# Performance work log

Hardware: AMD Instinct MI355X
Metric: run time of the kernel (lower is better)

The kernel has to match this reference:

```python
import jax, jax.numpy as jnp
import numpy as np

# Mamba-1.4B-like dims
BATCH, SEQ, HID = 1, 2048, 2048
INTER, STATE, DT_RANK, KCONV = 4096, 16, 128, 4


def setup_inputs() -> dict:
    key = jax.random.key(0)
    ks = jax.random.split(key, 8)
    f = jnp.float32
    return {
        "input_states": jax.random.normal(ks[0], (BATCH, SEQ, HID), f),
        "in_proj_w": jax.random.normal(ks[1], (HID, 2 * INTER), f) * (HID ** -0.5),
        "conv_w": jax.random.normal(ks[2], (INTER, 1, KCONV), f) * (KCONV ** -0.5),  # (O, I/groups=1, K) depthwise
        "conv_b": jnp.zeros((INTER,), f),
        "x_proj_w": jax.random.normal(ks[3], (INTER, DT_RANK + 2 * STATE), f) * (INTER ** -0.5),
        "dt_proj_w": jax.random.normal(ks[4], (DT_RANK, INTER), f) * (DT_RANK ** -0.5),
        "dt_proj_b": jax.random.normal(ks[5], (INTER,), f) * 0.1,
        "A_log": jnp.log(jnp.broadcast_to(jnp.arange(1, STATE + 1, dtype=f), (INTER, STATE))),
        "D": jnp.ones((INTER,), f),
        "out_proj_w": jax.random.normal(ks[6], (INTER, HID), f) * (INTER ** -0.5),
    }


def _mamba_forward(input_states, in_proj_w, conv_w, conv_b, x_proj_w,
                   dt_proj_w, dt_proj_b, A_log, D, out_proj_w):
    Bsz, L, _ = input_states.shape
    Idim, _, K = conv_w.shape
    N = A_log.shape[1]
    R = dt_proj_w.shape[0]

    proj = input_states @ in_proj_w                       # (B, L, 2I)
    hidden, gate = jnp.split(proj, 2, axis=-1)            # each (B, L, I)

    # depthwise causal conv over sequence (pad K-1, keep first L outputs)
    xc = jnp.swapaxes(hidden, 1, 2)                       # (B, I, L)
    xc = jax.lax.conv_general_dilated(
        xc, conv_w, window_strides=(1,), padding=((K - 1, K - 1),),
        feature_group_count=Idim)
    xc = xc[:, :, :L] + conv_b[None, :, None]
    u = jax.nn.silu(jnp.swapaxes(xc, 1, 2))               # (B, L, I)

    # input-dependent SSM params
    ssm_in = u @ x_proj_w                                 # (B, L, R + 2N)
    dt_in, Bc, Cc = jnp.split(ssm_in, [R, R + N], axis=-1)
    dt = jax.nn.softplus(dt_in @ dt_proj_w + dt_proj_b)   # (B, L, I)
    A = -jnp.exp(A_log)                                   # (I, N)

    def step(state, xs):
        dt_t, B_t, C_t, u_t = xs                          # (B,I) (B,N) (B,N) (B,I)
        dA = jnp.exp(dt_t[:, :, None] * A[None])          # (B, I, N)
        state = state * dA + (dt_t * u_t)[:, :, None] * B_t[:, None, :]
        y_t = jnp.einsum('bin,bn->bi', state, C_t)
        return state, y_t

    xs = (jnp.swapaxes(dt, 0, 1), jnp.swapaxes(Bc, 0, 1),
          jnp.swapaxes(Cc, 0, 1), jnp.swapaxes(u, 0, 1))
    state0 = jnp.zeros((Bsz, Idim, N), dt.dtype)
    _, ys = jax.lax.scan(step, state0, xs)                # (L, B, I)
    y = jnp.swapaxes(ys, 0, 1)                            # (B, L, I)

    y = (y + u * D) * jax.nn.silu(gate)
    return y @ out_proj_w                                 # (B, L, H)


def reference(input_states, in_proj_w, conv_w, conv_b, x_proj_w,
              dt_proj_w, dt_proj_b, A_log, D, out_proj_w):
    return _mamba_forward(input_states, in_proj_w, conv_w, conv_b, x_proj_w,
                          dt_proj_w, dt_proj_b, A_log, D, out_proj_w)
```

## Files before the change

kernel.cpp:

```cpp
#include <hip/hip_runtime.h>
#include <stdint.h>

#define LSEQ 2048
#define HID  2048
#define IDIM 4096
#define NSTATE 16
#define RRANK 128
#define GDIM 160

#define GCHUNK 64
#define TCHUNK (LSEQ / GCHUNK)

typedef _Float16 f16x8 __attribute__((ext_vector_type(8)));
typedef _Float16 f16x2 __attribute__((ext_vector_type(2)));
typedef float f32x4 __attribute__((ext_vector_type(4)));

#define GLOAD_LDS16(g, l) __builtin_amdgcn_global_load_lds( \
    (const __attribute__((address_space(1))) void*)(g),     \
    (__attribute__((address_space(3))) void*)(l), 16, 0, 0)

__device__ __forceinline__ float softplus_f(float x) {
    if (x > 20.f) return x;
    return log1pf(__expf(x));
}
__device__ __forceinline__ float silu_f(float x) {
    return x / (1.f + __expf(-x));
}

__device__ __forceinline__ void transpose_tile(const float* __restrict__ in,
                                               _Float16* __restrict__ out,
                                               int R, int C, int tr, int tc,
                                               _Float16 (*tile)[66]) {
    const int c0 = tc * 64, r0 = tr * 64;
    const int t = threadIdx.x;
    const int tx = t & 15, ty = t >> 4;
    const int ox = t & 7, oy = t >> 3;
    const bool full = (c0 + 64 <= C) && (r0 + 64 <= R);
    if (full) {
        #pragma unroll
        for (int j = 0; j < 4; ++j) {
            int r = ty + j * 16;
            float4 v = *(const float4*)(in + (long)(r0 + r) * C + c0 + tx * 4);
            tile[r][tx * 4 + 0] = (_Float16)v.x;
            tile[r][tx * 4 + 1] = (_Float16)v.y;
            tile[r][tx * 4 + 2] = (_Float16)v.z;
            tile[r][tx * 4 + 3] = (_Float16)v.w;
        }
        __syncthreads();
        #pragma unroll
        for (int j = 0; j < 2; ++j) {
            int c = oy + j * 32;
            f16x8 v;
            #pragma unroll
            for (int e = 0; e < 8; ++e) v[e] = tile[ox * 8 + e][c];
            *(f16x8*)(out + (long)(c0 + c) * R + r0 + ox * 8) = v;
        }
    } else {
        #pragma unroll
        for (int j = 0; j < 4; ++j) {
            int r = ty + j * 16;
            #pragma unroll
            for (int e = 0; e < 4; ++e) {
                int c = c0 + tx * 4 + e;
                float v = (r0 + r < R && c < C) ? in[(long)(r0 + r) * C + c] : 0.f;
                tile[r][tx * 4 + e] = (_Float16)v;
            }
        }
        __syncthreads();
        #pragma unroll
        for (int j = 0; j < 2; ++j) {
            int c = c0 + oy + j * 32;
            if (c < C) {
                #pragma unroll
                for (int e = 0; e < 8; ++e) {
                    int r = r0 + ox * 8 + e;
                    if (r < R) out[(long)c * R + r] = tile[ox * 8 + e][oy + j * 32];
                }
            }
        }
    }
}

__global__ __launch_bounds__(256)
void prep_kernel(const float* __restrict__ x_in, const float* __restrict__ w_in,
                 const float* __restrict__ xw, const float* __restrict__ dtw,
                 const float* __restrict__ ow,
                 _Float16* __restrict__ Xf, _Float16* __restrict__ Wt1,
                 _Float16* __restrict__ Wt2, _Float16* __restrict__ Wt3,
                 _Float16* __restrict__ Wt4) {
    __shared__ _Float16 tile[64][66];
    int b = blockIdx.x;
    if (b < 4096) { transpose_tile(w_in, Wt1, HID, 2 * IDIM, b / 128, b % 128, tile); return; }
    b -= 4096;
    if (b < 192) { transpose_tile(xw, Wt2, IDIM, GDIM, b / 3, b % 3, tile); return; }
    b -= 192;
    if (b < 128) { transpose_tile(dtw, Wt3, RRANK, IDIM, b / 64, b % 64, tile); return; }
    b -= 128;
    if (b < 2048) { transpose_tile(ow, Wt4, IDIM, HID, b / 32, b % 32, tile); return; }
    b -= 2048;
    long base = (long)b * 4096 + threadIdx.x * 16;
    #pragma unroll
    for (int h = 0; h < 2; ++h) {
        float4 a = *(const float4*)(x_in + base + h * 8);
        float4 c = *(const float4*)(x_in + base + h * 8 + 4);
        f16x8 v;
        v[0] = (_Float16)a.x; v[1] = (_Float16)a.y; v[2] = (_Float16)a.z; v[3] = (_Float16)a.w;
        v[4] = (_Float16)c.x; v[5] = (_Float16)c.y; v[6] = (_Float16)c.z; v[7] = (_Float16)c.w;
        *(f16x8*)(Xf + base + h * 8) = v;
    }
}

#define BM 128
#define BK 64

template <typename CT, int BN_, bool SOFTPLUS>
__global__ __launch_bounds__(256)
void gemm_bt_kernel(const _Float16* __restrict__ A, const _Float16* __restrict__ Bt,
                    CT* __restrict__ C, int M, int N, int K, int kc,
                    const float* __restrict__ bias) {
    constexpr int NI = BN_ / 32;
    constexpr int NISS_B = BN_ * 8 / 256;
    __shared__ _Float16 As[BM * BK];
    __shared__ _Float16 Bs[BN_ * BK];
    const int m0 = blockIdx.y * BM;
    const int n0 = blockIdx.x * BN_;
    const int t = threadIdx.x;
    const int wave = t >> 6;
    const int lane = t & 63;
    const int wm = wave >> 1, wn = wave & 1;
    const int lrow = lane & 15;
    const int quad = lane >> 4;
    const int sw8 = (lrow & 7) * 8;

    f32x4 acc[4][NI];
    #pragma unroll
    for (int mi = 0; mi < 4; ++mi)
        #pragma unroll
        for (int ni = 0; ni < NI; ++ni)
            #pragma unroll
            for (int r = 0; r < 4; ++r)
                acc[mi][ni][r] = 0.f;

    const int k_begin = blockIdx.z * kc;
    const _Float16* pA[4];
    #pragma unroll
    for (int j = 0; j < 4; ++j) {
        int s = j * 256 + t;
        int row = s >> 3;
        int ch = (s & 7) ^ (row & 7);
        pA[j] = A + (long)(m0 + row) * K + ch * 8 + k_begin;
    }
    const _Float16* pB[NISS_B];
    #pragma unroll
    for (int j = 0; j < NISS_B; ++j) {
        int s = j * 256 + t;
        int row = s >> 3;
        int ch = (s & 7) ^ (row & 7);
        pB[j] = Bt + (long)(n0 + row) * K + ch * 8 + k_begin;
    }

    for (int kk = 0; kk < kc; kk += BK) {
        #pragma unroll
        for (int j = 0; j < 4; ++j) {
            GLOAD_LDS16(pA[j], As + (j * 256 + wave * 64) * 8);
            pA[j] += BK;
        }
        #pragma unroll
        for (int j = 0; j < NISS_B; ++j) {
            GLOAD_LDS16(pB[j], Bs + (j * 256 + wave * 64) * 8);
            pB[j] += BK;
        }
        __syncthreads();

        #pragma unroll
        for (int h = 0; h < 2; ++h) {
            const int qoff = (h * 32 + quad * 8) ^ sw8;
            f16x8 af[4], bf[NI];
            #pragma unroll
            for (int mi = 0; mi < 4; ++mi)
                af[mi] = *(const f16x8*)(As + (wm * 64 + mi * 16 + lrow) * BK + qoff);
            #pragma unroll
            for (int ni = 0; ni < NI; ++ni)
                bf[ni] = *(const f16x8*)(Bs + (wn * (BN_ / 2) + ni * 16 + lrow) * BK + qoff);
            #pragma unroll
            for (int mi = 0; mi < 4; ++mi)
                #pragma unroll
                for (int ni = 0; ni < NI; ++ni)
                    acc[mi][ni] = __builtin_amdgcn_mfma_f32_16x16x32_f16(af[mi], bf[ni], acc[mi][ni], 0, 0, 0);
        }
        __syncthreads();
    }

    CT* Cz = C + (long)blockIdx.z * M * N;
    #pragma unroll
    for (int mi = 0; mi < 4; ++mi) {
        #pragma unroll
        for (int ni = 0; ni < NI; ++ni) {
            int col = n0 + wn * (BN_ / 2) + ni * 16 + lrow;
            if (col < N) {
                float bv = SOFTPLUS ? bias[col] : 0.f;
                #pragma unroll
                for (int r = 0; r < 4; ++r) {
                    int row = m0 + wm * 64 + mi * 16 + quad * 4 + r;
                    float v = acc[mi][ni][r];
                    if (SOFTPLUS) v = softplus_f(v + bv);
                    Cz[(long)row * N + col] = (CT)v;
                }
            }
        }
    }
}

__global__ void xproj_reduce_kernel(const float* __restrict__ part, float* __restrict__ ssm,
                                    _Float16* __restrict__ dtin) {
    int idx = blockIdx.x * 256 + threadIdx.x;
    if (idx >= LSEQ * GDIM) return;
    int t = idx / GDIM;
    int c = idx - t * GDIM;
    float v = 0.f;
    #pragma unroll
    for (int k = 0; k < 8; ++k)
        v += part[((long)k * LSEQ + t) * 256 + c];
    ssm[idx] = v;
    if (c < RRANK) dtin[t * RRANK + c] = (_Float16)v;
}

__global__ void opart_reduce_kernel(const float* __restrict__ part, float* __restrict__ out) {
    int idx = blockIdx.x * 256 + threadIdx.x;
    float4 a = ((const float4*)part)[idx];
    float4 b = ((const float4*)(part + (long)LSEQ * HID))[idx];
    ((float4*)out)[idx] = make_float4(a.x + b.x, a.y + b.y, a.z + b.z, a.w + b.w);
}

__global__ void conv_silu_kernel(const _Float16* __restrict__ proj, const float* __restrict__ w,
                                 const float* __restrict__ b, _Float16* __restrict__ u16) {
    int idx = blockIdx.x * 256 + threadIdx.x;
    int i0 = (idx & 511) * 8;
    int t0 = (idx >> 9) * 4;
    f16x8 r[7];
    #pragma unroll
    for (int k = 0; k < 7; ++k) {
        int tt = t0 - 3 + k;
        if (tt >= 0) r[k] = *(const f16x8*)(proj + (long)tt * (2 * IDIM) + i0);
        else         r[k] = f16x8{0,0,0,0,0,0,0,0};
    }
    float4 wv[8]; float bb[8];
    #pragma unroll
    for (int j = 0; j < 8; ++j) { wv[j] = ((const float4*)w)[i0 + j]; bb[j] = b[i0 + j]; }
    #pragma unroll
    for (int tt = 0; tt < 4; ++tt) {
        f16x8 res;
        #pragma unroll
        for (int j = 0; j < 8; ++j) {
            float a = bb[j] + (float)r[tt][j] * wv[j].x + (float)r[tt+1][j] * wv[j].y
                            + (float)r[tt+2][j] * wv[j].z + (float)r[tt+3][j] * wv[j].w;
            res[j] = (_Float16)(a / (1.f + __expf(-a)));
        }
        *(f16x8*)(u16 + (long)(t0 + tt) * IDIM + i0) = res;
    }
}

__global__ __launch_bounds__(256)
void scan_pass1_kernel(const _Float16* __restrict__ dtf, const float* __restrict__ ssm,
                       const _Float16* __restrict__ u16, const float* __restrict__ A_log,
                       _Float16* __restrict__ Pc, _Float16* __restrict__ Sc) {
    const int c = blockIdx.y;
    const int i0 = (blockIdx.x * 256 + threadIdx.x) * 2;

    __shared__ float Bs[TCHUNK * 16];
    for (int idx = threadIdx.x; idx < TCHUNK * 16; idx += 256) {
        int t = idx >> 4, n = idx & 15;
        Bs[idx] = ssm[(c * TCHUNK + t) * GDIM + RRANK + n];
    }
    __syncthreads();

    float A[2][16];
    #pragma unroll
    for (int ch = 0; ch < 2; ++ch) {
        const float4* Ap = (const float4*)(A_log + (long)(i0 + ch) * 16);
        #pragma unroll
        for (int q = 0; q < 4; ++q) {
            float4 v = Ap[q];
            A[ch][q * 4 + 0] = -__expf(v.x);
            A[ch][q * 4 + 1] = -__expf(v.y);
            A[ch][q * 4 + 2] = -__expf(v.z);
            A[ch][q * 4 + 3] = -__expf(v.w);
        }
    }

    float s[2][16], pr[2][16];
    #pragma unroll
    for (int ch = 0; ch < 2; ++ch)
        #pragma unroll
        for (int n = 0; n < 16; ++n) { s[ch][n] = 0.f; pr[ch][n] = 1.f; }

    long base = (long)c * TCHUNK * IDIM + i0;
    for (int t = 0; t < TCHUNK; ++t) {
        f16x2 dt2 = *(const f16x2*)(dtf + base + (long)t * IDIM);
        f16x2 u2  = *(const f16x2*)(u16 + base + (long)t * IDIM);
        #pragma unroll
        for (int ch = 0; ch < 2; ++ch) {
            float dt = (float)dt2[ch];
            float dtu = dt * (float)u2[ch];
            #pragma unroll
            for (int n = 0; n < 16; ++n) {
                float dA = __expf(dt * A[ch][n]);
                s[ch][n] = s[ch][n] * dA + dtu * Bs[t * 16 + n];
                pr[ch][n] *= dA;
            }
        }
    }

    long o = ((long)c * IDIM + i0) * 16;
    #pragma unroll
    for (int ch = 0; ch < 2; ++ch) {
        #pragma unroll
        for (int q = 0; q < 2; ++q) {
            f16x8 pv, sv;
            #pragma unroll
            for (int e = 0; e < 8; ++e) {
                pv[e] = (_Float16)pr[ch][q * 8 + e];
                sv[e] = (_Float16)s[ch][q * 8 + e];
            }
            *(f16x8*)(Pc + o + ch * 16 + q * 8) = pv;
            *(f16x8*)(Sc + o + ch * 16 + q * 8) = sv;
        }
    }
}

__global__ void scan_combine_kernel(const _Float16* __restrict__ Pc, _Float16* __restrict__ ScInit) {
    int tid = blockIdx.x * 256 + threadIdx.x;
    const long stride = (long)IDIM * 16;
    const long off = (long)tid * 2;
    f16x2 p4[4], s4[4];
    #pragma unroll
    for (int k = 0; k < 4; ++k) {
        p4[k] = *(const f16x2*)(Pc + (long)k * stride + off);
        s4[k] = *(const f16x2*)(ScInit + (long)k * stride + off);
    }
    float c0 = 0.f, c1 = 0.f;
    for (int g = 0; g < GCHUNK / 4; ++g) {
        f16x2 pc[4], sc[4];
        #pragma unroll
        for (int k = 0; k < 4; ++k) { pc[k] = p4[k]; sc[k] = s4[k]; }
        if (g + 1 < GCHUNK / 4) {
            #pragma unroll
            for (int k = 0; k < 4; ++k) {
                long o2 = (long)((g + 1) * 4 + k) * stride + off;
                p4[k] = *(const f16x2*)(Pc + o2);
                s4[k] = *(const f16x2*)(ScInit + o2);
            }
        }
        #pragma unroll
        for (int k = 0; k < 4; ++k) {
            long o = (long)(g * 4 + k) * stride + off;
            *(f16x2*)(ScInit + o) = f16x2{(_Float16)c0, (_Float16)c1};
            c0 = c0 * (float)pc[k][0] + (float)sc[k][0];
            c1 = c1 * (float)pc[k][1] + (float)sc[k][1];
        }
    }
}

__global__ __launch_bounds__(256)
void scan_pass3_kernel(const _Float16* __restrict__ dtf, const float* __restrict__ ssm,
                       const _Float16* __restrict__ u16, const _Float16* __restrict__ proj,
                       const float* __restrict__ A_log, const float* __restrict__ Dp,
                       const _Float16* __restrict__ Init, _Float16* __restrict__ y16) {
    const int c = blockIdx.y;
    const int i0 = (blockIdx.x * 256 + threadIdx.x) * 2;

    __shared__ float Bs[TCHUNK * 16];
    __shared__ float Cs[TCHUNK * 16];
    for (int idx = threadIdx.x; idx < TCHUNK * 16; idx += 256) {
        int t = idx >> 4, n = idx & 15;
        Bs[idx] = ssm[(c * TCHUNK + t) * GDIM + RRANK + n];
        Cs[idx] = ssm[(c * TCHUNK + t) * GDIM + RRANK + NSTATE + n];
    }
    __syncthreads();

    float A[2][16];
    #pragma unroll
    for (int ch = 0; ch < 2; ++ch) {
        const float4* Ap = (const float4*)(A_log + (long)(i0 + ch) * 16);
        #pragma unroll
        for (int q = 0; q < 4; ++q) {
            float4 v = Ap[q];
            A[ch][q * 4 + 0] = -__expf(v.x);
            A[ch][q * 4 + 1] = -__expf(v.y);
            A[ch][q * 4 + 2] = -__expf(v.z);
            A[ch][q * 4 + 3] = -__expf(v.w);
        }
    }
    float2 Dv = *(const float2*)(Dp + i0);

    float s[2][16];
    {
        long o = ((long)c * IDIM + i0) * 16;
        #pragma unroll
        for (int ch = 0; ch < 2; ++ch)
            #pragma unroll
            for (int q = 0; q < 2; ++q) {
                f16x8 v = *(const f16x8*)(Init + o + ch * 16 + q * 8);
                #pragma unroll
                for (int e = 0; e < 8; ++e) s[ch][q * 8 + e] = (float)v[e];
            }
    }

    long base = (long)c * TCHUNK * IDIM + i0;
    for (int t = 0; t < TCHUNK; ++t) {
        f16x2 dt2 = *(const f16x2*)(dtf + base + (long)t * IDIM);
        f16x2 u2  = *(const f16x2*)(u16 + base + (long)t * IDIM);
        int tg = c * TCHUNK + t;
        f16x2 g2 = *(const f16x2*)(proj + (long)tg * (2 * IDIM) + IDIM + i0);
        f16x2 res;
        #pragma unroll
        for (int ch = 0; ch < 2; ++ch) {
            float dt = (float)dt2[ch];
            float uv = (float)u2[ch];
            float dtu = dt * uv;
            float y = 0.f;
            #pragma unroll
            for (int n = 0; n < 16; ++n) {
                float dA = __expf(dt * A[ch][n]);
                s[ch][n] = s[ch][n] * dA + dtu * Bs[t * 16 + n];
                y += s[ch][n] * Cs[t * 16 + n];
            }
            float g = (float)g2[ch];
            float Dch = ch ? Dv.y : Dv.x;
            res[ch] = (_Float16)((y + uv * Dch) * silu_f(g));
        }
        *(f16x2*)(y16 + base + (long)t * IDIM) = res;
    }
}

extern "C" void kernel_launch(void* const* d_in, const int* in_sizes, int n_in,
                              void* d_out, int out_size, void* d_ws, size_t ws_size,
                              hipStream_t stream) {
    const float* x_in  = (const float*)d_in[0];
    const float* w_in  = (const float*)d_in[1];
    const float* cw    = (const float*)d_in[2];
    const float* cb    = (const float*)d_in[3];
    const float* xw    = (const float*)d_in[4];
    const float* dtw   = (const float*)d_in[5];
    const float* dtb   = (const float*)d_in[6];
    const float* alog  = (const float*)d_in[7];
    const float* Dp    = (const float*)d_in[8];
    const float* ow    = (const float*)d_in[9];
    float* out = (float*)d_out;

    char* p = (char*)d_ws;
    auto alloc = [&](size_t bytes) { char* r = p; p += (bytes + 255) & ~255ull; return r; };
    _Float16* Xf    = (_Float16*)alloc((size_t)LSEQ * HID * 2);
    _Float16* Wt1   = (_Float16*)alloc((size_t)2 * IDIM * HID * 2);
    _Float16* proj  = (_Float16*)alloc((size_t)LSEQ * 2 * IDIM * 2);
    _Float16* u16   = (_Float16*)alloc((size_t)LSEQ * IDIM * 2);
    _Float16* Wt2   = (_Float16*)alloc((size_t)256 * IDIM * 2);
    float*    ssm   = (float*)alloc((size_t)LSEQ * GDIM * 4);
    _Float16* dtin  = (_Float16*)alloc((size_t)LSEQ * RRANK * 2);
    _Float16* Wt3   = (_Float16*)alloc((size_t)IDIM * RRANK * 2);
    _Float16* dtf   = (_Float16*)alloc((size_t)LSEQ * IDIM * 2);
    _Float16* Wt4   = (_Float16*)alloc((size_t)HID * IDIM * 2);
    _Float16* y16   = (_Float16*)alloc((size_t)LSEQ * IDIM * 2);

    float* xpart = (float*)Wt1;
    _Float16* Pc = (_Float16*)Wt1;
    _Float16* Sc = Pc + (size_t)GCHUNK * IDIM * 16;
    float* opart = (float*)Wt1;

    prep_kernel<<<7488, 256, 0, stream>>>(x_in, w_in, xw, dtw, ow, Xf, Wt1, Wt2, Wt3, Wt4);
    gemm_bt_kernel<_Float16, 128, false><<<dim3(2 * IDIM / 128, LSEQ / BM, 1), 256, 0, stream>>>(
        Xf, Wt1, proj, LSEQ, 2 * IDIM, HID, HID, nullptr);
    conv_silu_kernel<<<(LSEQ / 4) * (IDIM / 8) / 256, 256, 0, stream>>>(proj, cw, cb, u16);
    gemm_bt_kernel<float, 128, false><<<dim3(2, LSEQ / BM, 8), 256, 0, stream>>>(
        u16, Wt2, xpart, LSEQ, 256, IDIM, IDIM / 8, nullptr);
    xproj_reduce_kernel<<<(LSEQ * GDIM + 255) / 256, 256, 0, stream>>>(xpart, ssm, dtin);
    gemm_bt_kernel<_Float16, 128, true><<<dim3(IDIM / 128, LSEQ / BM, 1), 256, 0, stream>>>(
        dtin, Wt3, dtf, LSEQ, IDIM, RRANK, RRANK, dtb);
    scan_pass1_kernel<<<dim3(IDIM / 512, GCHUNK), 256, 0, stream>>>(
        dtf, ssm, u16, alog, Pc, Sc);
    scan_combine_kernel<<<(IDIM * NSTATE / 2) / 256, 256, 0, stream>>>(Pc, Sc);
    scan_pass3_kernel<<<dim3(IDIM / 512, GCHUNK), 256, 0, stream>>>(
        dtf, ssm, u16, proj, alog, Dp, Sc, y16);
    gemm_bt_kernel<float, 128, false><<<dim3(HID / 128, LSEQ / BM, 2), 256, 0, stream>>>(
        y16, Wt4, opart, LSEQ, HID, IDIM, IDIM / 2, nullptr);
    opart_reduce_kernel<<<(LSEQ * HID / 4) / 256, 256, 0, stream>>>(opart, out);
}
```

Before: 470.6 us.

## Fuse pipeline stages into fewer kernels using software grid barriers

Merges the conv into the in-projection GEMM, the x-proj split-K reduction into its GEMM, the three scan passes into one kernel, and the out-proj reduction into its GEMM, each joined by an atomic-counter grid barrier. It also replaces the per-step running product of decay factors with a single exp of the summed dt, and stores out-proj partials in fp16. The goal is to cut kernel launch overhead and intermediate traffic. The catch is that the barriers need every block resident at once (1024 blocks for in-proj), which can deadlock or serialize. The fp16 partials also lower accuracy.

```diff
diff --git a/kernel.cpp b/kernel.cpp
--- a/kernel.cpp
+++ b/kernel.cpp
@@ -25,6 +25,17 @@
 }
 __device__ __forceinline__ float silu_f(float x) {
     return x / (1.f + __expf(-x));
+}
+
+__device__ __forceinline__ void grid_barrier(int* cnt, int expected) {
+    __syncthreads();
+    if (threadIdx.x == 0) {
+        __threadfence();
+        atomicAdd(cnt, 1);
+        while (__hip_atomic_load(cnt, __ATOMIC_ACQUIRE, __HIP_MEMORY_SCOPE_AGENT) < expected)
+            __builtin_amdgcn_s_sleep(2);
+    }
+    __syncthreads();
 }
 
 __device__ __forceinline__ void transpose_tile(const float* __restrict__ in,
@@ -87,9 +98,10 @@
                  const float* __restrict__ ow,
                  _Float16* __restrict__ Xf, _Float16* __restrict__ Wt1,
                  _Float16* __restrict__ Wt2, _Float16* __restrict__ Wt3,
-                 _Float16* __restrict__ Wt4) {
+                 _Float16* __restrict__ Wt4, int* __restrict__ ctr) {
     __shared__ _Float16 tile[64][66];
     int b = blockIdx.x;
+    if (b == 0 && threadIdx.x < 8) ctr[threadIdx.x] = 0;
     if (b < 4096) { transpose_tile(w_in, Wt1, HID, 2 * IDIM, b / 128, b % 128, tile); return; }
     b -= 4096;
     if (b < 192) { transpose_tile(xw, Wt2, IDIM, GDIM, b / 3, b % 3, tile); return; }
@@ -113,17 +125,14 @@
 #define BM 128
 #define BK 64
 
-template <typename CT, int BN_, bool SOFTPLUS>
-__global__ __launch_bounds__(256)
-void gemm_bt_kernel(const _Float16* __restrict__ A, const _Float16* __restrict__ Bt,
-                    CT* __restrict__ C, int M, int N, int K, int kc,
-                    const float* __restrict__ bias) {
-    constexpr int NI = BN_ / 32;
-    constexpr int NISS_B = BN_ * 8 / 256;
-    __shared__ _Float16 As[BM * BK];
-    __shared__ _Float16 Bs[BN_ * BK];
+template <typename CT, bool SOFTPLUS>
+__device__ __forceinline__
+void gemm_core(const _Float16* __restrict__ A, const _Float16* __restrict__ Bt,
+               CT* __restrict__ C, int M, int N, int K, int kc,
+               const float* __restrict__ bias,
+               _Float16* __restrict__ As, _Float16* __restrict__ Bs) {
     const int m0 = blockIdx.y * BM;
-    const int n0 = blockIdx.x * BN_;
+    const int n0 = blockIdx.x * 128;
     const int t = threadIdx.x;
     const int wave = t >> 6;
     const int lane = t & 63;
@@ -132,30 +141,24 @@
     const int quad = lane >> 4;
     const int sw8 = (lrow & 7) * 8;
 
-    f32x4 acc[4][NI];
+    f32x4 acc[4][4];
     #pragma unroll
     for (int mi = 0; mi < 4; ++mi)
         #pragma unroll
-        for (int ni = 0; ni < NI; ++ni)
+        for (int ni = 0; ni < 4; ++ni)
             #pragma unroll
             for (int r = 0; r < 4; ++r)
                 acc[mi][ni][r] = 0.f;
 
     const int k_begin = blockIdx.z * kc;
     const _Float16* pA[4];
+    const _Float16* pB[4];
     #pragma unroll
     for (int j = 0; j < 4; ++j) {
         int s = j * 256 + t;
         int row = s >> 3;
         int ch = (s & 7) ^ (row & 7);
         pA[j] = A + (long)(m0 + row) * K + ch * 8 + k_begin;
-    }
-    const _Float16* pB[NISS_B];
-    #pragma unroll
-    for (int j = 0; j < NISS_B; ++j) {
-        int s = j * 256 + t;
-        int row = s >> 3;
-        int ch = (s & 7) ^ (row & 7);
         pB[j] = Bt + (long)(n0 + row) * K + ch * 8 + k_begin;
     }
 
@@ -164,9 +167,6 @@
         for (int j = 0; j < 4; ++j) {
             GLOAD_LDS16(pA[j], As + (j * 256 + wave * 64) * 8);
             pA[j] += BK;
-        }
-        #pragma unroll
-        for (int j = 0; j < NISS_B; ++j) {
             GLOAD_LDS16(pB[j], Bs + (j * 256 + wave * 64) * 8);
             pB[j] += BK;
         }
@@ -175,17 +175,17 @@
         #pragma unroll
         for (int h = 0; h < 2; ++h) {
             const int qoff = (h * 32 + quad * 8) ^ sw8;
-            f16x8 af[4], bf[NI];
+            f16x8 af[4], bf[4];
             #pragma unroll
             for (int mi = 0; mi < 4; ++mi)
                 af[mi] = *(const f16x8*)(As + (wm * 64 + mi * 16 + lrow) * BK + qoff);
             #pragma unroll
-            for (int ni = 0; ni < NI; ++ni)
-                bf[ni] = *(const f16x8*)(Bs + (wn * (BN_ / 2) + ni * 16 + lrow) * BK + qoff);
+            for (int ni = 0; ni < 4; ++ni)
+                bf[ni] = *(const f16x8*)(Bs + (wn * 64 + ni * 16 + lrow) * BK + qoff);
             #pragma unroll
             for (int mi = 0; mi < 4; ++mi)
                 #pragma unroll
-                for (int ni = 0; ni < NI; ++ni)
+                for (int ni = 0; ni < 4; ++ni)
                     acc[mi][ni] = __builtin_amdgcn_mfma_f32_16x16x32_f16(af[mi], bf[ni], acc[mi][ni], 0, 0, 0);
         }
         __syncthreads();
@@ -195,8 +195,8 @@
     #pragma unroll
     for (int mi = 0; mi < 4; ++mi) {
         #pragma unroll
-        for (int ni = 0; ni < NI; ++ni) {
-            int col = n0 + wn * (BN_ / 2) + ni * 16 + lrow;
+        for (int ni = 0; ni < 4; ++ni) {
+            int col = n0 + wn * 64 + ni * 16 + lrow;
             if (col < N) {
                 float bv = SOFTPLUS ? bias[col] : 0.f;
                 #pragma unroll
@@ -211,30 +211,19 @@
     }
 }
 
-__global__ void xproj_reduce_kernel(const float* __restrict__ part, float* __restrict__ ssm,
-                                    _Float16* __restrict__ dtin) {
-    int idx = blockIdx.x * 256 + threadIdx.x;
-    if (idx >= LSEQ * GDIM) return;
-    int t = idx / GDIM;
-    int c = idx - t * GDIM;
-    float v = 0.f;
-    #pragma unroll
-    for (int k = 0; k < 8; ++k)
-        v += part[((long)k * LSEQ + t) * 256 + c];
-    ssm[idx] = v;
-    if (c < RRANK) dtin[t * RRANK + c] = (_Float16)v;
-}
-
-__global__ void opart_reduce_kernel(const float* __restrict__ part, float* __restrict__ out) {
-    int idx = blockIdx.x * 256 + threadIdx.x;
-    float4 a = ((const float4*)part)[idx];
-    float4 b = ((const float4*)(part + (long)LSEQ * HID))[idx];
-    ((float4*)out)[idx] = make_float4(a.x + b.x, a.y + b.y, a.z + b.z, a.w + b.w);
-}
-
-__global__ void conv_silu_kernel(const _Float16* __restrict__ proj, const float* __restrict__ w,
-                                 const float* __restrict__ b, _Float16* __restrict__ u16) {
-    int idx = blockIdx.x * 256 + threadIdx.x;
+__global__ __launch_bounds__(256, 4)
+void inproj_conv_kernel(const _Float16* __restrict__ Xf, const _Float16* __restrict__ Wt1,
+                        _Float16* __restrict__ proj, const float* __restrict__ cw,
+                        const float* __restrict__ cb, _Float16* __restrict__ u16,
+                        int* __restrict__ ctr) {
+    __shared__ _Float16 As[BM * BK];
+    __shared__ _Float16 Bs[128 * BK];
+    gemm_core<_Float16, false>(Xf, Wt1, proj, LSEQ, 2 * IDIM, HID, HID, nullptr, As, Bs);
+
+    grid_barrier(ctr, 1024);
+
+    int bid = blockIdx.y * gridDim.x + blockIdx.x;
+    int idx = bid * 256 + threadIdx.x;
     int i0 = (idx & 511) * 8;
     int t0 = (idx >> 9) * 4;
     f16x8 r[7];
@@ -246,7 +235,7 @@
     }
     float4 wv[8]; float bb[8];
     #pragma unroll
-    for (int j = 0; j < 8; ++j) { wv[j] = ((const float4*)w)[i0 + j]; bb[j] = b[i0 + j]; }
+    for (int j = 0; j < 8; ++j) { wv[j] = ((const float4*)cw)[i0 + j]; bb[j] = cb[i0 + j]; }
     #pragma unroll
     for (int tt = 0; tt < 4; ++tt) {
         f16x8 res;
@@ -261,16 +250,78 @@
 }
 
 __global__ __launch_bounds__(256)
-void scan_pass1_kernel(const _Float16* __restrict__ dtf, const float* __restrict__ ssm,
-                       const _Float16* __restrict__ u16, const float* __restrict__ A_log,
-                       _Float16* __restrict__ Pc, _Float16* __restrict__ Sc) {
-    const int c = blockIdx.y;
-    const int i0 = (blockIdx.x * 256 + threadIdx.x) * 2;
-
-    __shared__ float Bs[TCHUNK * 16];
+void xproj_kernel(const _Float16* __restrict__ u16, const _Float16* __restrict__ Wt2,
+                  float* __restrict__ xpart, float* __restrict__ ssm,
+                  _Float16* __restrict__ dtin, int* __restrict__ ctr) {
+    __shared__ _Float16 As[BM * BK];
+    __shared__ _Float16 Bs[128 * BK];
+    gemm_core<float, false>(u16, Wt2, xpart, LSEQ, 256, IDIM, IDIM / 8, nullptr, As, Bs);
+
+    grid_barrier(ctr, 256);
+
+    int bid = (blockIdx.z * gridDim.y + blockIdx.y) * gridDim.x + blockIdx.x;
+    for (int k = bid * 256 + threadIdx.x; k < LSEQ * GDIM; k += 256 * 256) {
+        int t = k / GDIM;
+        int c = k - t * GDIM;
+        float v = 0.f;
+        #pragma unroll
+        for (int z = 0; z < 8; ++z)
+            v += xpart[((long)z * LSEQ + t) * 256 + c];
+        ssm[k] = v;
+        if (c < RRANK) dtin[t * RRANK + c] = (_Float16)v;
+    }
+}
+
+__global__ __launch_bounds__(256)
+void dtproj_kernel(const _Float16* __restrict__ dtin, const _Float16* __restrict__ Wt3,
+                   _Float16* __restrict__ dtf, const float* __restrict__ dtb) {
+    __shared__ _Float16 As[BM * BK];
+    __shared__ _Float16 Bs[128 * BK];
+    gemm_core<_Float16, true>(dtin, Wt3, dtf, LSEQ, IDIM, RRANK, RRANK, dtb, As, Bs);
+}
+
+__global__ __launch_bounds__(256, 2)
+void outproj_kernel(const _Float16* __restrict__ y16, const _Float16* __restrict__ Wt4,
+                    _Float16* __restrict__ opart, float* __restrict__ out,
+                    int* __restrict__ ctr) {
+    __shared__ _Float16 As[BM * BK];
+    __shared__ _Float16 Bs[128 * BK];
+    gemm_core<_Float16, false>(y16, Wt4, opart, LSEQ, HID, IDIM, IDIM / 2, nullptr, As, Bs);
+
+    grid_barrier(ctr, 512);
+
+    int bid = (blockIdx.z * gridDim.y + blockIdx.y) * gridDim.x + blockIdx.x;
+    long base = ((long)bid * 256 + threadIdx.x) * 32;
+    #pragma unroll
+    for (int j = 0; j < 4; ++j) {
+        f16x8 a = *(const f16x8*)(opart + base + j * 8);
+        f16x8 b = *(const f16x8*)(opart + (long)LSEQ * HID + base + j * 8);
+        float4 o0 = make_float4((float)a[0] + (float)b[0], (float)a[1] + (float)b[1],
+                                (float)a[2] + (float)b[2], (float)a[3] + (float)b[3]);
+        float4 o1 = make_float4((float)a[4] + (float)b[4], (float)a[5] + (float)b[5],
+                                (float)a[6] + (float)b[6], (float)a[7] + (float)b[7]);
+        *(float4*)(out + base + j * 8) = o0;
+        *(float4*)(out + base + j * 8 + 4) = o1;
+    }
+}
+
+__global__ __launch_bounds__(256, 2)
+void scan_mega_kernel(const _Float16* __restrict__ dtf, const float* __restrict__ ssm,
+                      const _Float16* __restrict__ u16, const _Float16* __restrict__ proj,
+                      const float* __restrict__ A_log, const float* __restrict__ Dp,
+                      _Float16* __restrict__ Pc, _Float16* __restrict__ Sc,
+                      _Float16* __restrict__ y16, int* __restrict__ ctr1, int* __restrict__ ctr2) {
+    __shared__ float Bsh[TCHUNK * 16];
+    __shared__ float Csh[TCHUNK * 16];
+    const int bx = blockIdx.x;
+    const int c = bx >> 3;
+    const int isl = bx & 7;
+    const int i0 = (isl * 256 + threadIdx.x) * 2;
+
     for (int idx = threadIdx.x; idx < TCHUNK * 16; idx += 256) {
         int t = idx >> 4, n = idx & 15;
-        Bs[idx] = ssm[(c * TCHUNK + t) * GDIM + RRANK + n];
+        Bsh[idx] = ssm[(c * TCHUNK + t) * GDIM + RRANK + n];
+        Csh[idx] = ssm[(c * TCHUNK + t) * GDIM + RRANK + NSTATE + n];
     }
     __syncthreads();
 
@@ -288,148 +339,124 @@
         }
     }
 
-    float s[2][16], pr[2][16];
-    #pragma unroll
-    for (int ch = 0; ch < 2; ++ch)
-        #pragma unroll
-        for (int n = 0; n < 16; ++n) { s[ch][n] = 0.f; pr[ch][n] = 1.f; }
-
-    long base = (long)c * TCHUNK * IDIM + i0;
-    for (int t = 0; t < TCHUNK; ++t) {
-        f16x2 dt2 = *(const f16x2*)(dtf + base + (long)t * IDIM);
-        f16x2 u2  = *(const f16x2*)(u16 + base + (long)t * IDIM);
+    {
+        float s[2][16];
+        float sumdt[2] = {0.f, 0.f};
+        #pragma unroll
+        for (int ch = 0; ch < 2; ++ch)
+            #pragma unroll
+            for (int n = 0; n < 16; ++n) s[ch][n] = 0.f;
+
+        long base = (long)c * TCHUNK * IDIM + i0;
+        for (int t = 0; t < TCHUNK; ++t) {
+            f16x2 dt2 = *(const f16x2*)(dtf + base + (long)t * IDIM);
+            f16x2 u2  = *(const f16x2*)(u16 + base + (long)t * IDIM);
+            #pragma unroll
+            for (int ch = 0; ch < 2; ++ch) {
+                float dt = (float)dt2[ch];
+                float dtu = dt * (float)u2[ch];
+                sumdt[ch] += dt;
+                #pragma unroll
+                for (int n = 0; n < 16; ++n) {
+                    float dA = __expf(dt * A[ch][n]);
+                    s[ch][n] = s[ch][n] * dA + dtu * Bsh[t * 16 + n];
+                }
+            }
+        }
+        long o = ((long)c * IDIM + i0) * 16;
         #pragma unroll
         for (int ch = 0; ch < 2; ++ch) {
-            float dt = (float)dt2[ch];
-            float dtu = dt * (float)u2[ch];
-            #pragma unroll
-            for (int n = 0; n < 16; ++n) {
-                float dA = __expf(dt * A[ch][n]);
-                s[ch][n] = s[ch][n] * dA + dtu * Bs[t * 16 + n];
-                pr[ch][n] *= dA;
-            }
-        }
-    }
-
-    long o = ((long)c * IDIM + i0) * 16;
-    #pragma unroll
-    for (int ch = 0; ch < 2; ++ch) {
-        #pragma unroll
-        for (int q = 0; q < 2; ++q) {
-            f16x8 pv, sv;
-            #pragma unroll
-            for (int e = 0; e < 8; ++e) {
-                pv[e] = (_Float16)pr[ch][q * 8 + e];
-                sv[e] = (_Float16)s[ch][q * 8 + e];
-            }
-            *(f16x8*)(Pc + o + ch * 16 + q * 8) = pv;
-            *(f16x8*)(Sc + o + ch * 16 + q * 8) = sv;
-        }
-    }
-}
-
-__global__ void scan_combine_kernel(const _Float16* __restrict__ Pc, _Float16* __restrict__ ScInit) {
-    int tid = blockIdx.x * 256 + threadIdx.x;
-    const long stride = (long)IDIM * 16;
-    const long off = (long)tid * 2;
-    f16x2 p4[4], s4[4];
-    #pragma unroll
-    for (int k = 0; k < 4; ++k) {
-        p4[k] = *(const f16x2*)(Pc + (long)k * stride + off);
-        s4[k] = *(const f16x2*)(ScInit + (long)k * stride + off);
-    }
-    float c0 = 0.f, c1 = 0.f;
-    for (int g = 0; g < GCHUNK / 4; ++g) {
-        f16x2 pc[4], sc[4];
-        #pragma unroll
-        for (int k = 0; k < 4; ++k) { pc[k] = p4[k]; sc[k] = s4[k]; }
-        if (g + 1 < GCHUNK / 4) {
+            #pragma unroll
+            for (int q = 0; q < 2; ++q) {
+                f16x8 pv, sv;
+                #pragma unroll
+                for (int e = 0; e < 8; ++e) {
+                    pv[e] = (_Float16)__expf(A[ch][q * 8 + e] * sumdt[ch]);
+                    sv[e] = (_Float16)s[ch][q * 8 + e];
+                }
+                *(f16x8*)(Pc + o + ch * 16 + q * 8) = pv;
+                *(f16x8*)(Sc + o + ch * 16 + q * 8) = sv;
+            }
+        }
+    }
+
+    grid_barrier(ctr1, 512);
+
+    {
+        int pair = bx * 256 + threadIdx.x;
+        if (pair < IDIM * 16 / 2) {
+            const long stride = (long)IDIM * 16;
+            const long off = (long)pair * 2;
+            f16x2 p4[4], s4[4];
             #pragma unroll
             for (int k = 0; k < 4; ++k) {
-                long o2 = (long)((g + 1) * 4 + k) * stride + off;
-                p4[k] = *(const f16x2*)(Pc + o2);
-                s4[k] = *(const f16x2*)(ScInit + o2);
-            }
-        }
-        #pragma unroll
-        for (int k = 0; k < 4; ++k) {
-            long o = (long)(g * 4 + k) * stride + off;
-            *(f16x2*)(ScInit + o) = f16x2{(_Float16)c0, (_Float16)c1};
-            c0 = c0 * (float)pc[k][0] + (float)sc[k][0];
-            c1 = c1 * (float)pc[k][1] + (float)sc[k][1];
-        }
-    }
-}
-
-__global__ __launch_bounds__(256)
-void scan_pass3_kernel(const _Float16* __restrict__ dtf, const float* __restrict__ ssm,
-                       const _Float16* __restrict__ u16, const _Float16* __restrict__ proj,
-                       const float* __restrict__ A_log, const float* __restrict__ Dp,
-                       const _Float16* __restrict__ Init, _Float16* __restrict__ y16) {
-    const int c = blockIdx.y;
-    const int i0 = (blockIdx.x * 256 + threadIdx.x) * 2;
-
-    __shared__ float Bs[TCHUNK * 16];
-    __shared__ float Cs[TCHUNK * 16];
-    for (int idx = threadIdx.x; idx < TCHUNK * 16; idx += 256) {
-        int t = idx >> 4, n = idx & 15;
-        Bs[idx] = ssm[(c * TCHUNK + t) * GDIM + RRANK + n];
-        Cs[idx] = ssm[(c * TCHUNK + t) * GDIM + RRANK + NSTATE + n];
-    }
-    __syncthreads();
-
-    float A[2][16];
-    #pragma unroll
-    for (int ch = 0; ch < 2; ++ch) {
-        const float4* Ap = (const float4*)(A_log + (long)(i0 + ch) * 16);
-        #pragma unroll
-        for (int q = 0; q < 4; ++q) {
-            float4 v = Ap[q];
-            A[ch][q * 4 + 0] = -__expf(v.x);
-            A[ch][q * 4 + 1] = -__expf(v.y);
-            A[ch][q * 4 + 2] = -__expf(v.z);
-            A[ch][q * 4 + 3] = -__expf(v.w);
-        }
-    }
-    float2 Dv = *(const float2*)(Dp + i0);
-
-    float s[2][16];
+                p4[k] = *(const f16x2*)(Pc + (long)k * stride + off);
+                s4[k] = *(const f16x2*)(Sc + (long)k * stride + off);
+            }
+            float c0 = 0.f, c1 = 0.f;
+            for (int g = 0; g < GCHUNK / 4; ++g) {
+                f16x2 pc[4], sc[4];
+                #pragma unroll
+                for (int k = 0; k < 4; ++k) { pc[k] = p4[k]; sc[k] = s4[k]; }
+                if (g + 1 < GCHUNK / 4) {
+                    #pragma unroll
+                    for (int k = 0; k < 4; ++k) {
+                        long o2 = (long)((g + 1) * 4 + k) * stride + off;
+                        p4[k] = *(const f16x2*)(Pc + o2);
+                        s4[k] = *(const f16x2*)(Sc + o2);
+                    }
+                }
+                #pragma unroll
+                for (int k = 0; k < 4; ++k) {
+                    long o = (long)(g * 4 + k) * stride + off;
+                    *(f16x2*)(Sc + o) = f16x2{(_Float16)c0, (_Float16)c1};
+                    c0 = c0 * (float)pc[k][0] + (float)sc[k][0];
+                    c1 = c1 * (float)pc[k][1] + (float)sc[k][1];
+                }
+            }
+        }
+    }
+
+    grid_barrier(ctr2, 512);
+
     {
+        float2 Dv = *(const float2*)(Dp + i0);
+        float s[2][16];
         long o = ((long)c * IDIM + i0) * 16;
         #pragma unroll
         for (int ch = 0; ch < 2; ++ch)
             #pragma unroll
             for (int q = 0; q < 2; ++q) {
-                f16x8 v = *(const f16x8*)(Init + o + ch * 16 + q * 8);
+                f16x8 v = *(const f16x8*)(Sc + o + ch * 16 + q * 8);
                 #pragma unroll
                 for (int e = 0; e < 8; ++e) s[ch][q * 8 + e] = (float)v[e];
             }
-    }
-
-    long base = (long)c * TCHUNK * IDIM + i0;
-    for (int t = 0; t < TCHUNK; ++t) {
-        f16x2 dt2 = *(const f16x2*)(dtf + base + (long)t * IDIM);
-        f16x2 u2  = *(const f16x2*)(u16 + base + (long)t * IDIM);
-        int tg = c * TCHUNK + t;
-        f16x2 g2 = *(const f16x2*)(proj + (long)tg * (2 * IDIM) + IDIM + i0);
-        f16x2 res;
-        #pragma unroll
-        for (int ch = 0; ch < 2; ++ch) {
-            float dt = (float)dt2[ch];
-            float uv = (float)u2[ch];
-            float dtu = dt * uv;
-            float y = 0.f;
-            #pragma unroll
-            for (int n = 0; n < 16; ++n) {
-                float dA = __expf(dt * A[ch][n]);
-                s[ch][n] = s[ch][n] * dA + dtu * Bs[t * 16 + n];
-                y += s[ch][n] * Cs[t * 16 + n];
-            }
-            float g = (float)g2[ch];
-            float Dch = ch ? Dv.y : Dv.x;
-            res[ch] = (_Float16)((y + uv * Dch) * silu_f(g));
-        }
-        *(f16x2*)(y16 + base + (long)t * IDIM) = res;
+
+        long base = (long)c * TCHUNK * IDIM + i0;
+        for (int t = 0; t < TCHUNK; ++t) {
+            f16x2 dt2 = *(const f16x2*)(dtf + base + (long)t * IDIM);
+            f16x2 u2  = *(const f16x2*)(u16 + base + (long)t * IDIM);
+            int tg = c * TCHUNK + t;
+            f16x2 g2 = *(const f16x2*)(proj + (long)tg * (2 * IDIM) + IDIM + i0);
+            f16x2 res;
+            #pragma unroll
+            for (int ch = 0; ch < 2; ++ch) {
+                float dt = (float)dt2[ch];
+                float uv = (float)u2[ch];
+                float dtu = dt * uv;
+                float y = 0.f;
+                #pragma unroll
+                for (int n = 0; n < 16; ++n) {
+                    float dA = __expf(dt * A[ch][n]);
+                    s[ch][n] = s[ch][n] * dA + dtu * Bsh[t * 16 + n];
+                    y += s[ch][n] * Csh[t * 16 + n];
+                }
+                float g = (float)g2[ch];
+                float Dch = ch ? Dv.y : Dv.x;
+                res[ch] = (_Float16)((y + uv * Dch) * silu_f(g));
+            }
+            *(f16x2*)(y16 + base + (long)t * IDIM) = res;
+        }
     }
 }
 
@@ -461,27 +488,21 @@
     _Float16* dtf   = (_Float16*)alloc((size_t)LSEQ * IDIM * 2);
     _Float16* Wt4   = (_Float16*)alloc((size_t)HID * IDIM * 2);
     _Float16* y16   = (_Float16*)alloc((size_t)LSEQ * IDIM * 2);
+    int*      ctr   = (int*)alloc(256);
 
     float* xpart = (float*)Wt1;
     _Float16* Pc = (_Float16*)Wt1;
     _Float16* Sc = Pc + (size_t)GCHUNK * IDIM * 16;
-    float* opart = (float*)Wt1;
-
-    prep_kernel<<<7488, 256, 0, stream>>>(x_in, w_in, xw, dtw, ow, Xf, Wt1, Wt2, Wt3, Wt4);
-    gemm_bt_kernel<_Float16, 128, false><<<dim3(2 * IDIM / 128, LSEQ / BM, 1), 256, 0, stream>>>(
-        Xf, Wt1, proj, LSEQ, 2 * IDIM, HID, HID, nullptr);
-    conv_silu_kernel<<<(LSEQ / 4) * (IDIM / 8) / 256, 256, 0, stream>>>(proj, cw, cb, u16);
-    gemm_bt_kernel<float, 128, false><<<dim3(2, LSEQ / BM, 8), 256, 0, stream>>>(
-        u16, Wt2, xpart, LSEQ, 256, IDIM, IDIM / 8, nullptr);
-    xproj_reduce_kernel<<<(LSEQ * GDIM + 255) / 256, 256, 0, stream>>>(xpart, ssm, dtin);
-    gemm_bt_kernel<_Float16, 128, true><<<dim3(IDIM / 128, LSEQ / BM, 1), 256, 0, stream>>>(
-        dtin, Wt3, dtf, LSEQ, IDIM, RRANK, RRANK, dtb);
-    scan_pass1_kernel<<<dim3(IDIM / 512, GCHUNK), 256, 0, stream>>>(
-        dtf, ssm, u16, alog, Pc, Sc);
-    scan_combine_kernel<<<(IDIM * NSTATE / 2) / 256, 256, 0, stream>>>(Pc, Sc);
-    scan_pass3_kernel<<<dim3(IDIM / 512, GCHUNK), 256, 0, stream>>>(
-        dtf, ssm, u16, proj, alog, Dp, Sc, y16);
-    gemm_bt_kernel<float, 128, false><<<dim3(HID / 128, LSEQ / BM, 2), 256, 0, stream>>>(
-        y16, Wt4, opart, LSEQ, HID, IDIM, IDIM / 2, nullptr);
-    opart_reduce_kernel<<<(LSEQ * HID / 4) / 256, 256, 0, stream>>>(opart, out);
-}
+    _Float16* opart = (_Float16*)Wt1;
+
+    prep_kernel<<<7488, 256, 0, stream>>>(x_in, w_in, xw, dtw, ow, Xf, Wt1, Wt2, Wt3, Wt4, ctr);
+    inproj_conv_kernel<<<dim3(2 * IDIM / 128, LSEQ / BM), 256, 0, stream>>>(
+        Xf, Wt1, proj, cw, cb, u16, ctr + 0);
+    xproj_kernel<<<dim3(2, LSEQ / BM, 8), 256, 0, stream>>>(
+        u16, Wt2, xpart, ssm, dtin, ctr + 1);
+    dtproj_kernel<<<dim3(IDIM / 128, LSEQ / BM), 256, 0, stream>>>(dtin, Wt3, dtf, dtb);
+    scan_mega_kernel<<<512, 256, 0, stream>>>(
+        dtf, ssm, u16, proj, alog, Dp, Pc, Sc, y16, ctr + 2, ctr + 3);
+    outproj_kernel<<<dim3(HID / 128, LSEQ / BM, 2), 256, 0, stream>>>(
+        y16, Wt4, opart, out, ctr + 4);
+}
```

Result: slower. 1.189 ms (+152.6%).
